# Performance work log

Hardware: AMD Instinct MI355X
Metric: run time of the kernel (lower is better)

## Reference

```python
import jax, jax.numpy as jnp
import numpy as np

B, L, K = 16384, 512, 4
N_ITERS = 5
EPS = 1e-08
NOISE_SCALE = 0.01


def setup_inputs() -> dict:
    key = jax.random.key(0)
    k1, k2, k3 = jax.random.split(key, 3)
    return {
        "windows": jax.random.normal(k1, (B, L), dtype=jnp.float32),
        "init_centers": jax.random.normal(k2, (K,), dtype=jnp.float32),
        "init_scales": jnp.ones((K,), dtype=jnp.float32),
        "init_weights": jnp.ones((K,), dtype=jnp.float32) / K,
        "prior_p_param": -jnp.ones((1,), dtype=jnp.float32),
        "weights_param": jnp.zeros((1, L), dtype=jnp.float32),
        "blend": jnp.zeros((1,), dtype=jnp.float32),
        "noise": jax.random.normal(k3, (B, K), dtype=jnp.float32),
    }


def _em(windows, init_centers, init_scales, init_weights,
        prior_p_param, weights_param, blend, noise):
    # windows: [B, L]
    data_mean = jnp.mean(windows, axis=-1, keepdims=True)          # [B, 1]
    data_std = jnp.std(windows, axis=-1, keepdims=True, ddof=1)    # [B, 1] (torch.std is unbiased)
    prior_var = jnp.var(windows, axis=-1, keepdims=True, ddof=1)   # [B, 1]

    # _initialize_parameters (noise passed in as standard normal, scaled here)
    mu = init_centers[None, :] * data_std + data_mean + noise * data_std * NOISE_SCALE  # [B, K]
    sigma = jnp.abs(init_scales)[None, :] * data_std                                    # [B, K]
    w = jnp.broadcast_to(init_weights[None, :], mu.shape)                               # [B, K]

    # _get_parameters
    weights = jnp.exp(weights_param)[..., None]   # [1, L, 1]
    blender = jax.nn.sigmoid(blend)               # [1]
    prior_p = jax.nn.sigmoid(prior_p_param)       # [1]

    g = None
    for _ in range(N_ITERS):
        # E-step: responsibilities via stable softmax over components
        log_w = jnp.log((w + EPS) / (sigma + EPS))[:, None, :]                 # [B, 1, K]
        z = (windows[..., None] - mu[:, None, :]) / (sigma[:, None, :] + EPS)  # [B, L, K]
        log_mix = -0.5 * z * z + log_w                                         # [B, L, K]
        g = jax.nn.softmax(log_mix, axis=-1)                                   # [B, L, K]

        # M-step
        wg = g * weights                                   # [B, L, K]
        sum_g = jnp.maximum(jnp.sum(wg, axis=-2), EPS)     # [B, K]
        w = sum_g + prior_p
        w = w / jnp.sum(w, axis=-1, keepdims=True)
        data_mu = jnp.sum(wg * windows[..., None], axis=-2) / sum_g            # [B, K]
        mu = data_mu * blender + data_mean * (1.0 - blender)                   # [B, K]
        diff = windows[..., None] - mu[:, None, :]                             # [B, L, K]
        data_var = jnp.sum(wg * diff * diff, axis=-2) / sum_g                  # [B, K]
        var = data_var * blender + prior_var * (1.0 - blender)
        sigma = jnp.sqrt(var + EPS)

    return g, w, mu, sigma


def reference(windows, init_centers, init_scales, init_weights,
              prior_p_param, weights_param, blend, noise):
    return _em(windows, init_centers, init_scales, init_weights,
               prior_p_param, weights_param, blend, noise)
```

## Files before the change

### kernel.cpp

```cpp
#include <hip/hip_runtime.h>
#include <math.h>


constexpr int Bn = 16384;
constexpr int Ln = 512;
constexpr int Kn = 4;
constexpr int NITER = 5;
constexpr float EPSf = 1e-8f;
constexpr float NOISEf = 0.01f;
constexpr float LOG2E = 1.4426950408889634f;

__device__ __forceinline__ float wred(float v) {
#pragma unroll
    for (int m = 32; m >= 1; m >>= 1) v += __shfl_xor(v, m, 64);
    return v;
}

__device__ __forceinline__ float frcp(float v) { return __builtin_amdgcn_rcpf(v); }

struct RowState {
    float x[8], xx[8], wl[8];
    float mu[4], w[4], inv_se[4], sig[4];
    float mean, prior_var, blender, omb, prior_p;
};

template <bool LAST>
__device__ __forceinline__ void em_iter(RowState& st, float* __restrict__ gout, int lane) {
    float A2[4], B2[4], C2[4];
#pragma unroll
    for (int k = 0; k < 4; ++k) {
        float is2 = st.inv_se[k] * st.inv_se[k];
        float lw2 = __log2f((st.w[k] + EPSf) * st.inv_se[k]);
        A2[k] = (-0.5f * LOG2E) * is2;
        B2[k] = (LOG2E * st.mu[k]) * is2;
        C2[k] = fmaf((-0.5f * LOG2E) * (st.mu[k] * st.mu[k]), is2, lw2);
    }

    float S0[4] = {0,0,0,0}, S1[4] = {0,0,0,0}, S2[4] = {0,0,0,0};
#pragma unroll
    for (int j = 0; j < 8; ++j) {
        float e[4];
        float esum = 0.f;
#pragma unroll
        for (int k = 0; k < 4; ++k) {
            float lm = fmaf(A2[k], st.xx[j], fmaf(B2[k], st.x[j], C2[k]));
            e[k] = __builtin_amdgcn_exp2f(lm);
            esum += e[k];
        }
        float inv = frcp(esum);
        float wls = st.wl[j] * inv;
#pragma unroll
        for (int k = 0; k < 4; ++k) {
            float wg = e[k] * wls;
            S0[k] += wg;
            S1[k] = fmaf(wg, st.x[j], S1[k]);
            S2[k] = fmaf(wg, st.xx[j], S2[k]);
        }
        if (LAST) {
            float4 g4 = make_float4(e[0] * inv, e[1] * inv, e[2] * inv, e[3] * inv);
            *(float4*)(gout + (size_t)(lane + 64 * j) * 4) = g4;
        }
    }
#pragma unroll
    for (int k = 0; k < 4; ++k) {
        S0[k] = wred(S0[k]);
        S1[k] = wred(S1[k]);
        S2[k] = wred(S2[k]);
    }

    float wn[4], wsum = 0.f;
#pragma unroll
    for (int k = 0; k < 4; ++k) {
        float sg = fmaxf(S0[k], EPSf);
        float rsg = frcp(sg);
        float dmu = S1[k] * rsg;
        float mun = fmaf(st.blender, dmu, st.omb * st.mean);
        float num = fmaf(mun * mun, S0[k], fmaf(-2.f * mun, S1[k], S2[k]));
        float dv = fmaxf(num * rsg, 0.f);
        float var = fmaf(st.blender, dv, st.omb * st.prior_var);
        float sgn = sqrtf(var + EPSf);
        st.mu[k] = mun;
        st.sig[k] = sgn;
        st.inv_se[k] = frcp(sgn + EPSf);
        wn[k] = sg + st.prior_p;
        wsum += wn[k];
    }
    float invws = frcp(wsum);
#pragma unroll
    for (int k = 0; k < 4; ++k) st.w[k] = wn[k] * invws;
}

__global__ __launch_bounds__(256, 4) void em_kernel(
    const float* __restrict__ windows,
    const float* __restrict__ centers,
    const float* __restrict__ scales,
    const float* __restrict__ iweights,
    const float* __restrict__ prior_p_param,
    const float* __restrict__ weights_param,
    const float* __restrict__ blend,
    const float* __restrict__ noise,
    float* __restrict__ out_g,
    float* __restrict__ out_w,
    float* __restrict__ out_mu,
    float* __restrict__ out_sigma)
{
    const int lane = threadIdx.x & 63;
    const int wv = threadIdx.x >> 6;
    const int b = blockIdx.x * 4 + wv;

    RowState st;
    const float* __restrict__ xr = windows + (size_t)b * Ln;
#pragma unroll
    for (int j = 0; j < 8; ++j) {
        float v = xr[lane + 64 * j];
        st.x[j] = v;
        st.xx[j] = v * v;
        st.wl[j] = __expf(weights_param[lane + 64 * j]);
    }

    float s = 0.f, ss = 0.f;
#pragma unroll
    for (int j = 0; j < 8; ++j) { s += st.x[j]; ss += st.xx[j]; }
    s = wred(s); ss = wred(ss);
    st.mean = s * (1.0f / Ln);
    float var1 = fmaxf((ss - s * st.mean) * (1.0f / (Ln - 1)), 0.f);
    const float sd = sqrtf(var1);
    st.prior_var = var1;

    st.prior_p = 1.f / (1.f + __expf(-prior_p_param[0]));
    st.blender = 1.f / (1.f + __expf(-blend[0]));
    st.omb = 1.f - st.blender;

    const float4 nz = *(const float4*)(noise + (size_t)b * 4);
    const float nzv[4] = { nz.x, nz.y, nz.z, nz.w };

#pragma unroll
    for (int k = 0; k < 4; ++k) {
        st.mu[k] = fmaf(centers[k], sd, st.mean) + nzv[k] * sd * NOISEf;
        float sg0 = fabsf(scales[k]) * sd;
        st.sig[k] = sg0;
        st.w[k] = iweights[k];
        st.inv_se[k] = frcp(sg0 + EPSf);
    }

    float* gout = out_g + (size_t)b * Ln * Kn;
    for (int it = 0; it < NITER - 1; ++it)
        em_iter<false>(st, gout, lane);
    em_iter<true>(st, gout, lane);

    if (lane == 0) {
        *(float4*)(out_w     + (size_t)b * 4) = make_float4(st.w[0], st.w[1], st.w[2], st.w[3]);
        *(float4*)(out_mu    + (size_t)b * 4) = make_float4(st.mu[0], st.mu[1], st.mu[2], st.mu[3]);
        *(float4*)(out_sigma + (size_t)b * 4) = make_float4(st.sig[0], st.sig[1], st.sig[2], st.sig[3]);
    }
}

extern "C" void kernel_launch(void* const* d_in, const int* in_sizes, int n_in,
                              void* d_out, int out_size, void* d_ws, size_t ws_size,
                              hipStream_t stream) {
    const float* windows       = (const float*)d_in[0];
    const float* init_centers  = (const float*)d_in[1];
    const float* init_scales   = (const float*)d_in[2];
    const float* init_weights  = (const float*)d_in[3];
    const float* prior_p_param = (const float*)d_in[4];
    const float* weights_param = (const float*)d_in[5];
    const float* blend         = (const float*)d_in[6];
    const float* noise         = (const float*)d_in[7];

    float* out       = (float*)d_out;
    float* out_g     = out;
    float* out_w     = out_g + (size_t)Bn * Ln * Kn;
    float* out_mu    = out_w + (size_t)Bn * Kn;
    float* out_sigma = out_mu + (size_t)Bn * Kn;

    dim3 grid(Bn / 4);
    dim3 block(256);
    hipLaunchKernelGGL(em_kernel, grid, block, 0, stream,
                       windows, init_centers, init_scales, init_weights,
                       prior_p_param, weights_param, blend, noise,
                       out_g, out_w, out_mu, out_sigma);
}
```

Baseline: 218.5 us.

## Derive fourth component sums from precomputed totals and use DPP reductions

Because responsibilities sum to one per element, the weighted sums for the fourth component are now the precomputed row totals of weight, weight*x and weight*x² minus the other three components' sums. This drops one component's accumulation and its wave reductions in every iteration. Wave reductions also switch from xor shuffles to DPP row operations followed by a readlane of the last lane. Subtracting totals risks cancellation error when the fourth component's weight is small.

Result: faster. 213.8 us (-2.1%).

```diff
diff --git a/kernel.cpp b/kernel.cpp
--- a/kernel.cpp
+++ b/kernel.cpp
@@ -10,18 +10,29 @@
 constexpr float NOISEf = 0.01f;
 constexpr float LOG2E = 1.4426950408889634f;
 
-__device__ __forceinline__ float wred(float v) {
-#pragma unroll
-    for (int m = 32; m >= 1; m >>= 1) v += __shfl_xor(v, m, 64);
-    return v;
-}
-
 __device__ __forceinline__ float frcp(float v) { return __builtin_amdgcn_rcpf(v); }
+
+template <int CTRL>
+__device__ __forceinline__ float dpp_add(float v) {
+    int t = __builtin_amdgcn_update_dpp(0, __float_as_int(v), CTRL, 0xF, 0xF, true);
+    return v + __int_as_float(t);
+}
+
+__device__ __forceinline__ float wred_total(float v) {
+    v = dpp_add<0x111>(v);
+    v = dpp_add<0x112>(v);
+    v = dpp_add<0x114>(v);
+    v = dpp_add<0x118>(v);
+    v = dpp_add<0x142>(v);
+    v = dpp_add<0x143>(v);
+    return __int_as_float(__builtin_amdgcn_readlane(__float_as_int(v), 63));
+}
 
 struct RowState {
     float x[8], xx[8], wl[8];
     float mu[4], w[4], inv_se[4], sig[4];
     float mean, prior_var, blender, omb, prior_p;
+    float W0, W1, W2;
 };
 
 template <bool LAST>
@@ -36,7 +47,7 @@
         C2[k] = fmaf((-0.5f * LOG2E) * (st.mu[k] * st.mu[k]), is2, lw2);
     }
 
-    float S0[4] = {0,0,0,0}, S1[4] = {0,0,0,0}, S2[4] = {0,0,0,0};
+    float S0[3] = {0,0,0}, S1[3] = {0,0,0}, S2[3] = {0,0,0};
 #pragma unroll
     for (int j = 0; j < 8; ++j) {
         float e[4];
@@ -49,33 +60,39 @@
         }
         float inv = frcp(esum);
         float wls = st.wl[j] * inv;
-#pragma unroll
-        for (int k = 0; k < 4; ++k) {
-            float wg = e[k] * wls;
-            S0[k] += wg;
-            S1[k] = fmaf(wg, st.x[j], S1[k]);
-            S2[k] = fmaf(wg, st.xx[j], S2[k]);
+        float wlsx = wls * st.x[j];
+        float wlsxx = wls * st.xx[j];
+#pragma unroll
+        for (int k = 0; k < 3; ++k) {
+            S0[k] = fmaf(e[k], wls,   S0[k]);
+            S1[k] = fmaf(e[k], wlsx,  S1[k]);
+            S2[k] = fmaf(e[k], wlsxx, S2[k]);
         }
         if (LAST) {
             float4 g4 = make_float4(e[0] * inv, e[1] * inv, e[2] * inv, e[3] * inv);
             *(float4*)(gout + (size_t)(lane + 64 * j) * 4) = g4;
         }
     }
+
+    float T0[4], T1[4], T2[4];
+#pragma unroll
+    for (int k = 0; k < 3; ++k) {
+        T0[k] = wred_total(S0[k]);
+        T1[k] = wred_total(S1[k]);
+        T2[k] = wred_total(S2[k]);
+    }
+    T0[3] = st.W0 - T0[0] - T0[1] - T0[2];
+    T1[3] = st.W1 - T1[0] - T1[1] - T1[2];
+    T2[3] = st.W2 - T2[0] - T2[1] - T2[2];
+
+    float wn[4], wsum = 0.f;
 #pragma unroll
     for (int k = 0; k < 4; ++k) {
-        S0[k] = wred(S0[k]);
-        S1[k] = wred(S1[k]);
-        S2[k] = wred(S2[k]);
-    }
-
-    float wn[4], wsum = 0.f;
-#pragma unroll
-    for (int k = 0; k < 4; ++k) {
-        float sg = fmaxf(S0[k], EPSf);
+        float sg = fmaxf(T0[k], EPSf);
         float rsg = frcp(sg);
-        float dmu = S1[k] * rsg;
+        float dmu = T1[k] * rsg;
         float mun = fmaf(st.blender, dmu, st.omb * st.mean);
-        float num = fmaf(mun * mun, S0[k], fmaf(-2.f * mun, S1[k], S2[k]));
+        float num = fmaf(mun * mun, T0[k], fmaf(-2.f * mun, T1[k], T2[k]));
         float dv = fmaxf(num * rsg, 0.f);
         float var = fmaf(st.blender, dv, st.omb * st.prior_var);
         float sgn = sqrtf(var + EPSf);
@@ -118,10 +135,21 @@
         st.wl[j] = __expf(weights_param[lane + 64 * j]);
     }
 
-    float s = 0.f, ss = 0.f;
-#pragma unroll
-    for (int j = 0; j < 8; ++j) { s += st.x[j]; ss += st.xx[j]; }
-    s = wred(s); ss = wred(ss);
+    float s = 0.f, ss = 0.f, w0 = 0.f, w1 = 0.f, w2 = 0.f;
+#pragma unroll
+    for (int j = 0; j < 8; ++j) {
+        s += st.x[j];
+        ss += st.xx[j];
+        w0 += st.wl[j];
+        w1 = fmaf(st.wl[j], st.x[j], w1);
+        w2 = fmaf(st.wl[j], st.xx[j], w2);
+    }
+    s = wred_total(s);
+    ss = wred_total(ss);
+    st.W0 = wred_total(w0);
+    st.W1 = wred_total(w1);
+    st.W2 = wred_total(w2);
+
     st.mean = s * (1.0f / Ln);
     float var1 = fmaxf((ss - s * st.mean) * (1.0f / (Ln - 1)), 0.f);
     const float sd = sqrtf(var1);
```
